# Performance work log

Measured on AMD Instinct MI355X. Metric: run time of the kernel, lower is better.

## Reference

```python
import jax, jax.numpy as jnp
import numpy as np

N = 50000        # nodes
E = 1600000      # edges (before self loops)
IN = 256         # in_channels
C = 32           # hidden_channels (per head)
H = 4            # heads
OUT = 64         # out_channels
NEG_SLOPE = 0.2  # PyG GATConv default


def setup_inputs() -> dict:
    key = jax.random.key(0)
    ks = jax.random.split(key, 8)
    x = jax.random.normal(ks[0], (N, IN), dtype=jnp.float32)
    edge_index = jax.random.randint(ks[1], (2, E), 0, N, dtype=jnp.int64)
    s = 0.05
    W = jax.random.normal(ks[2], (IN, H * C), dtype=jnp.float32) * s
    att_src = jax.random.normal(ks[3], (H, C), dtype=jnp.float32) * s
    att_dst = jax.random.normal(ks[4], (H, C), dtype=jnp.float32) * s
    bias = jnp.zeros((H * C,), dtype=jnp.float32)
    lin_W = jax.random.normal(ks[5], (H * C, OUT), dtype=jnp.float32) * s
    lin_b = jnp.zeros((OUT,), dtype=jnp.float32)
    return {"x": x, "edge_index": edge_index, "W": W, "att_src": att_src,
            "att_dst": att_dst, "bias": bias, "lin_W": lin_W, "lin_b": lin_b}


def reference(x, edge_index, W, att_src, att_dst, bias, lin_W, lin_b):
    # Linear transform per head: [N, H, C]
    h = (x @ W).reshape(N, H, C)
    # Per-node attention halves (PyG GATConv): [N, H]
    a_src = jnp.einsum('nhc,hc->nh', h, att_src)
    a_dst = jnp.einsum('nhc,hc->nh', h, att_dst)
    # Add self loops (PyG default add_self_loops=True)
    loop = jnp.arange(N, dtype=edge_index.dtype)
    src = jnp.concatenate([edge_index[0], loop])  # message source j
    dst = jnp.concatenate([edge_index[1], loop])  # message target i
    # Edge attention logits: LeakyReLU(a_src[j] + a_dst[i])  -> [E+N, H]
    e = jax.nn.leaky_relu(a_src[src] + a_dst[dst], negative_slope=NEG_SLOPE)
    # Segment softmax over incoming edges of each destination node
    emax = jax.lax.stop_gradient(jax.ops.segment_max(e, dst, num_segments=N))
    emax = jnp.where(jnp.isfinite(emax), emax, 0.0)
    ex = jnp.exp(e - emax[dst])
    denom = jax.ops.segment_sum(ex, dst, num_segments=N)
    alpha = ex / denom[dst]  # [E+N, H]; self loops guarantee denom > 0
    # Weighted scatter-sum of source features: [N, H, C]
    msg = alpha[:, :, None] * h[src]
    agg = jax.ops.segment_sum(msg, dst, num_segments=N)
    out = agg.reshape(N, H * C) + bias  # concat heads + bias
    out = jax.nn.elu(out)
    return out @ lin_W + lin_b
```

## Files before the change

kernel.cpp:

```cpp
#include <hip/hip_runtime.h>
#include <cstdint>
#include <cstddef>

#define N_NODES 50000
#define N_EDGES 1600000
#define TOT_E   (N_EDGES + N_NODES)
#define IN_DIM  256
#define HC      128
#define NHEAD   4
#define OUT_DIM 64

#define SHIFT   7
#define BSZ     128
#define NBUK    ((N_NODES + BSZ - 1) / BSZ)
#define CHUNK   2048
#define EPT     8
#define NCHUNK  ((TOT_E + CHUNK - 1) / CHUNK)
#define CAP     6144
#define QCAP    1792

#define XPAD 264
#define HPAD 132
#define K1_NB ((N_NODES + 63) / 64)

typedef __attribute__((ext_vector_type(8))) short bf16x8;
typedef __attribute__((ext_vector_type(4))) float f32x4;

static __device__ __forceinline__ uint16_t f2bf(float f) {
    uint32_t u = __float_as_uint(f);
    uint32_t r = (u + 0x7fffu + ((u >> 16) & 1u)) >> 16;
    return (uint16_t)r;
}
static __device__ __forceinline__ float bf_lo(uint32_t u) {
    return __uint_as_float(u << 16);
}
static __device__ __forceinline__ float bf_hi(uint32_t u) {
    return __uint_as_float(u & 0xffff0000u);
}

__global__ __launch_bounds__(256) void w2bf(const float* __restrict__ W,
                                            uint16_t* __restrict__ wt,
                                            int* __restrict__ gcur) {
    int idx = blockIdx.x * 256 + threadIdx.x;
    int n = idx >> 8, k = idx & 255;
    wt[idx] = f2bf(W[(size_t)k * HC + n]);
    if (idx < NBUK) gcur[idx] = 0;
}

__global__ __launch_bounds__(256) void k1p3(const float* __restrict__ x,
                                            const uint16_t* __restrict__ wt,
                                            const float* __restrict__ att_src,
                                            const float* __restrict__ att_dst,
                                            uint16_t* __restrict__ hb,
                                            float* __restrict__ a_src,
                                            float* __restrict__ a_dst,
                                            const int* __restrict__ ei,
                                            int* __restrict__ gcur,
                                            uint32_t* __restrict__ binned) {
    __shared__ char smem[64 * 528];
    __shared__ float att_s[HC], att_d[HC];
    const int tid = threadIdx.x;

    if (blockIdx.x < K1_NB) {
        uint16_t* xs = (uint16_t*)smem;
        float*    hs = (float*)smem;
        const int wave = tid >> 6;
        const int lane = tid & 63;
        const int m    = lane & 15;
        const int q    = lane >> 4;
        const int row0 = blockIdx.x * 64;

        if (tid < HC) { att_s[tid] = att_src[tid]; att_d[tid] = att_dst[tid]; }

        for (int i = tid * 4; i < 64 * IN_DIM; i += 1024) {
            int r = i >> 8, c = i & 255;
            int gr = row0 + r;
            float4 v = make_float4(0.f, 0.f, 0.f, 0.f);
            if (gr < N_NODES) v = *(const float4*)(x + (size_t)gr * IN_DIM + c);
            uint32_t lo = (uint32_t)f2bf(v.x) | ((uint32_t)f2bf(v.y) << 16);
            uint32_t hi = (uint32_t)f2bf(v.z) | ((uint32_t)f2bf(v.w) << 16);
            *(uint2*)(xs + r * XPAD + c) = make_uint2(lo, hi);
        }
        __syncthreads();

        f32x4 acc[8];
        #pragma unroll
        for (int t = 0; t < 8; ++t) acc[t] = (f32x4){0.f, 0.f, 0.f, 0.f};

        const int arow = wave * 16 + m;
        #pragma unroll
        for (int ks = 0; ks < IN_DIM; ks += 32) {
            bf16x8 a = *(const bf16x8*)(xs + arow * XPAD + ks + q * 8);
            #pragma unroll
            for (int t = 0; t < 8; ++t) {
                bf16x8 b = *(const bf16x8*)(wt + (size_t)(t * 16 + m) * IN_DIM + ks + q * 8);
                acc[t] = __builtin_amdgcn_mfma_f32_16x16x32_bf16(a, b, acc[t], 0, 0, 0);
            }
        }
        __syncthreads();

        #pragma unroll
        for (int t = 0; t < 8; ++t)
            #pragma unroll
            for (int r = 0; r < 4; ++r)
                hs[(wave * 16 + q * 4 + r) * HPAD + t * 16 + m] = acc[t][r];
        __syncthreads();

        for (int i = tid * 4; i < 64 * HC; i += 1024) {
            int r = i >> 7, c = i & 127;
            if (row0 + r < N_NODES) {
                float4 v = *(const float4*)(hs + r * HPAD + c);
                uint32_t lo = (uint32_t)f2bf(v.x) | ((uint32_t)f2bf(v.y) << 16);
                uint32_t hi = (uint32_t)f2bf(v.z) | ((uint32_t)f2bf(v.w) << 16);
                *(uint2*)(hb + (size_t)(row0 + r) * HC + c) = make_uint2(lo, hi);
            }
        }
        {
            int r = tid >> 2, hd = tid & 3;
            if (row0 + r < N_NODES) {
                float s = 0.f, d = 0.f;
                #pragma unroll
                for (int j = 0; j < 32; ++j) {
                    float v = hs[r * HPAD + hd * 32 + j];
                    s = fmaf(v, att_s[hd * 32 + j], s);
                    d = fmaf(v, att_d[hd * 32 + j], d);
                }
                a_src[(row0 + r) * NHEAD + hd] = s;
                a_dst[(row0 + r) * NHEAD + hd] = d;
            }
        }
    } else {
        int* hist = (int*)smem;
        int* lcur = hist + NBUK;
        for (int i = tid; i < NBUK; i += 256) hist[i] = 0;
        __syncthreads();

        uint32_t wreg[EPT];
        const int base = (blockIdx.x - K1_NB) * CHUNK;
        #pragma unroll
        for (int k = 0; k < EPT; ++k) {
            int e = base + k * 256 + tid;
            uint32_t word = 0xFFFFFFFFu;
            if (e < TOT_E) {
                int src, dst;
                if (e < N_EDGES) { src = ei[e]; dst = ei[N_EDGES + e]; }
                else             { src = e - N_EDGES; dst = src; }
                int b = dst >> SHIFT;
                word = (uint32_t)src | ((uint32_t)(dst & (BSZ - 1)) << 16)
                     | ((uint32_t)b << 23);
                atomicAdd(&hist[b], 1);
            }
            wreg[k] = word;
        }
        __syncthreads();
        for (int i = tid; i < NBUK; i += 256) {
            int c = hist[i];
            lcur[i] = c ? atomicAdd(&gcur[i], c) : 0;
        }
        __syncthreads();
        #pragma unroll
        for (int k = 0; k < EPT; ++k) {
            uint32_t word = wreg[k];
            if (word != 0xFFFFFFFFu) {
                int b = (int)(word >> 23);
                int pos = atomicAdd(&lcur[b], 1);
                if (pos < CAP) binned[(size_t)b * CAP + pos] = word;
            }
        }
    }
}

__global__ __launch_bounds__(256) void q4_agg(const uint32_t* __restrict__ binned,
                                              const int* __restrict__ gcur,
                                              const uint32_t* __restrict__ hb32,
                                              const float* __restrict__ a_src,
                                              const float* __restrict__ a_dst,
                                              const float* __restrict__ bias,
                                              uint32_t* __restrict__ actb) {
    __shared__ uint32_t ewb[QCAP];
    __shared__ uint32_t ew2[QCAP];
    __shared__ int ncnt[32], nbeg[32], ncur[32];
    __shared__ int tot;
    const int b   = blockIdx.x >> 2;
    const int sub = blockIdx.x & 3;
    const int tid = threadIdx.x;

    int cnt = gcur[b];
    if (cnt > CAP) cnt = CAP;
    if (tid == 0) tot = 0;
    if (tid < 32) ncnt[tid] = 0;
    __syncthreads();

    const uint32_t* bb = binned + (size_t)b * CAP;
    for (int i = tid; i < cnt; i += 256) {
        uint32_t word = bb[i];
        int dl = (word >> 16) & 127;
        if ((dl >> 5) == sub) {
            int pos = atomicAdd(&tot, 1);
            if (pos < QCAP) ewb[pos] = word;
            atomicAdd(&ncnt[dl & 31], 1);
        }
    }
    __syncthreads();
    int T = tot;
    if (T > QCAP) T = QCAP;

    if (tid < 32) {
        int v = ncnt[tid];
        int inc = v;
        #pragma unroll
        for (int d = 1; d < 32; d <<= 1) {
            int t = __shfl_up(inc, d, 64);
            if (tid >= d) inc += t;
        }
        nbeg[tid] = inc - v;
        ncur[tid] = inc - v;
    }
    __syncthreads();
    for (int i = tid; i < T; i += 256) {
        uint32_t word = ewb[i];
        int ln  = (word >> 16) & 31;
        int pos = atomicAdd(&ncur[ln], 1);
        ew2[pos] = word & 0xFFFFu;
    }
    __syncthreads();

    const int wave = tid >> 6;
    const int lane = tid & 63;
    const int head = lane >> 4;
    const uint32_t* hbl = hb32 + lane;
    const float*    ash = a_src + head;

    for (int k = 0; k < 8; ++k) {
        const int ln   = wave * 8 + k;
        const int node = b * BSZ + sub * 32 + ln;
        if (node >= N_NODES) continue;

        const float ad = a_dst[node * NHEAD + head];
        int p = nbeg[ln];
        const int end = p + ncnt[ln];

        float l = 0.f, acc0 = 0.f, acc1 = 0.f;

        for (; p + 4 <= end; p += 4) {
            int s0 = (int)ew2[p + 0];
            int s1 = (int)ew2[p + 1];
            int s2 = (int)ew2[p + 2];
            int s3 = (int)ew2[p + 3];
            float e0 = ash[s0 * NHEAD] + ad;
            float e1 = ash[s1 * NHEAD] + ad;
            float e2 = ash[s2 * NHEAD] + ad;
            float e3 = ash[s3 * NHEAD] + ad;
            uint32_t u0 = hbl[(size_t)s0 * 64];
            uint32_t u1 = hbl[(size_t)s1 * 64];
            uint32_t u2 = hbl[(size_t)s2 * 64];
            uint32_t u3 = hbl[(size_t)s3 * 64];
            e0 = fmaxf(e0, 0.2f * e0);
            e1 = fmaxf(e1, 0.2f * e1);
            e2 = fmaxf(e2, 0.2f * e2);
            e3 = fmaxf(e3, 0.2f * e3);
            float w0 = __expf(e0), w1 = __expf(e1);
            float w2 = __expf(e2), w3 = __expf(e3);
            l += (w0 + w1) + (w2 + w3);
            acc0 = fmaf(w0, bf_lo(u0), acc0);
            acc1 = fmaf(w0, bf_hi(u0), acc1);
            acc0 = fmaf(w1, bf_lo(u1), acc0);
            acc1 = fmaf(w1, bf_hi(u1), acc1);
            acc0 = fmaf(w2, bf_lo(u2), acc0);
            acc1 = fmaf(w2, bf_hi(u2), acc1);
            acc0 = fmaf(w3, bf_lo(u3), acc0);
            acc1 = fmaf(w3, bf_hi(u3), acc1);
        }
        for (; p < end; ++p) {
            int s = (int)ew2[p];
            float e = ash[s * NHEAD] + ad;
            e = fmaxf(e, 0.2f * e);
            float w = __expf(e);
            uint32_t u = hbl[(size_t)s * 64];
            l += w;
            acc0 = fmaf(w, bf_lo(u), acc0);
            acc1 = fmaf(w, bf_hi(u), acc1);
        }

        const int c0 = lane << 1;
        float inv = 1.f / l;
        float o0 = acc0 * inv + bias[c0];
        float o1 = acc1 * inv + bias[c0 + 1];
        o0 = (o0 > 0.f) ? o0 : (__expf(o0) - 1.f);
        o1 = (o1 > 0.f) ? o1 : (__expf(o1) - 1.f);
        actb[(size_t)node * 64 + lane] = (uint32_t)f2bf(o0) | ((uint32_t)f2bf(o1) << 16);
    }
}

__global__ __launch_bounds__(512) void k7_out(const uint32_t* __restrict__ actb,
                                              const float* __restrict__ linW,
                                              const float* __restrict__ linb,
                                              float* __restrict__ out) {
    __shared__ float sW[HC * OUT_DIM];
    __shared__ float srow[32 * HC];
    const int tid   = threadIdx.x;
    const int node0 = blockIdx.x * 32;

    for (int i = tid * 4; i < HC * OUT_DIM; i += 512 * 4)
        *(float4*)(sW + i) = *(const float4*)(linW + i);
    {
        int i = tid * 4;
        int r = i >> 6, cw = i & 63;
        int node = node0 + r;
        uint4 v = make_uint4(0, 0, 0, 0);
        if (node < N_NODES) v = *(const uint4*)(actb + (size_t)node * 64 + cw);
        float* d = srow + r * HC + cw * 2;
        d[0] = bf_lo(v.x); d[1] = bf_hi(v.x);
        d[2] = bf_lo(v.y); d[3] = bf_hi(v.y);
        d[4] = bf_lo(v.z); d[5] = bf_hi(v.z);
        d[6] = bf_lo(v.w); d[7] = bf_hi(v.w);
    }
    __syncthreads();

    const int r    = tid >> 4;
    const int colb = (tid & 15) << 2;
    float4 acc = *(const float4*)(linb + colb);
    const float* rp = srow + r * HC;

    #pragma unroll
    for (int k = 0; k < HC; k += 4) {
        float4 xv = *(const float4*)(rp + k);
        float4 w0 = *(const float4*)(sW + (k + 0) * OUT_DIM + colb);
        float4 w1 = *(const float4*)(sW + (k + 1) * OUT_DIM + colb);
        float4 w2 = *(const float4*)(sW + (k + 2) * OUT_DIM + colb);
        float4 w3 = *(const float4*)(sW + (k + 3) * OUT_DIM + colb);
        acc.x += xv.x * w0.x; acc.x += xv.y * w1.x; acc.x += xv.z * w2.x; acc.x += xv.w * w3.x;
        acc.y += xv.x * w0.y; acc.y += xv.y * w1.y; acc.y += xv.z * w2.y; acc.y += xv.w * w3.y;
        acc.z += xv.x * w0.z; acc.z += xv.y * w1.z; acc.z += xv.z * w2.z; acc.z += xv.w * w3.z;
        acc.w += xv.x * w0.w; acc.w += xv.y * w1.w; acc.w += xv.z * w2.w; acc.w += xv.w * w3.w;
    }

    int node = node0 + r;
    if (node < N_NODES)
        *(float4*)(out + (size_t)node * OUT_DIM + colb) = acc;
}

extern "C" void kernel_launch(void* const* d_in, const int* in_sizes, int n_in,
                              void* d_out, int out_size, void* d_ws, size_t ws_size,
                              hipStream_t stream) {
    (void)in_sizes; (void)n_in; (void)out_size; (void)ws_size;
    const float* x       = (const float*)d_in[0];
    const int*   ei      = (const int*)d_in[1];
    const float* W       = (const float*)d_in[2];
    const float* att_src = (const float*)d_in[3];
    const float* att_dst = (const float*)d_in[4];
    const float* bias    = (const float*)d_in[5];
    const float* linW    = (const float*)d_in[6];
    const float* linb    = (const float*)d_in[7];
    float*       out     = (float*)d_out;

    char*  ws  = (char*)d_ws;
    size_t off = 0;
    auto alloc = [&](size_t bytes) -> void* {
        void* p = ws + off;
        off += (bytes + 255) & ~(size_t)255;
        return p;
    };
    uint16_t* hb     = (uint16_t*)alloc((size_t)N_NODES * HC * 2);
    uint16_t* wt     = (uint16_t*)alloc((size_t)HC * IN_DIM * 2);
    uint32_t* actb   = (uint32_t*)alloc((size_t)N_NODES * 64 * 4);
    float*    a_src  = (float*)alloc((size_t)N_NODES * NHEAD * 4);
    float*    a_dst  = (float*)alloc((size_t)N_NODES * NHEAD * 4);
    int*      gcur   = (int*)alloc((size_t)NBUK * 4);
    uint32_t* binned = (uint32_t*)alloc((size_t)NBUK * CAP * 4);

    w2bf<<<(HC * IN_DIM) / 256, 256, 0, stream>>>(W, wt, gcur);
    k1p3<<<K1_NB + NCHUNK, 256, 0, stream>>>(x, wt, att_src, att_dst,
                                             hb, a_src, a_dst,
                                             ei, gcur, binned);
    q4_agg<<<NBUK * 4, 256, 0, stream>>>(binned, gcur, (const uint32_t*)hb,
                                         a_src, a_dst, bias, actb);
    k7_out<<<(N_NODES + 31) / 32, 512, 0, stream>>>(actb, linW, linb, out);
}
```

Measured before the change: 248.8 us.

## Vectorize aggregation per lane across 4 nodes and use MFMA for output linear

The aggregation kernel now processes four destination nodes per wave at once: each 16-lane group owns a node and each lane gathers 16 bytes (8 bf16 channels) per source, with edge lists padded to multiples of 4 and masked weights instead of a scalar tail loop. Source indices are stored as 16-bit values so four can be read with one LDS load. The final linear layer is rewritten to use bf16 MFMA 16x16x32 with linW split into hi and lo bf16 parts to keep near-fp32 accuracy, replacing the scalar FP32 LDS GEMM. The trade-offs are divergence, since every group runs to the wave's maximum degree, and extra weight preprocessing work in w2bf.

```diff
diff --git a/kernel.cpp b/kernel.cpp
--- a/kernel.cpp
+++ b/kernel.cpp
@@ -23,8 +23,12 @@
 #define HPAD 132
 #define K1_NB ((N_NODES + 63) / 64)
 
+#define W2_GEMM_BLK ((HC * IN_DIM) / 256)
+#define W2_LIN_BLK  ((OUT_DIM * HC) / 256)
+
 typedef __attribute__((ext_vector_type(8))) short bf16x8;
 typedef __attribute__((ext_vector_type(4))) float f32x4;
+typedef __attribute__((ext_vector_type(4))) unsigned short u16x4;
 
 static __device__ __forceinline__ uint16_t f2bf(float f) {
     uint32_t u = __float_as_uint(f);
@@ -39,12 +43,24 @@
 }
 
 __global__ __launch_bounds__(256) void w2bf(const float* __restrict__ W,
+                                            const float* __restrict__ linW,
                                             uint16_t* __restrict__ wt,
+                                            uint16_t* __restrict__ lwt,
                                             int* __restrict__ gcur) {
-    int idx = blockIdx.x * 256 + threadIdx.x;
-    int n = idx >> 8, k = idx & 255;
-    wt[idx] = f2bf(W[(size_t)k * HC + n]);
-    if (idx < NBUK) gcur[idx] = 0;
+    if (blockIdx.x < W2_GEMM_BLK) {
+        int idx = blockIdx.x * 256 + threadIdx.x;
+        int n = idx >> 8, k = idx & 255;
+        wt[idx] = f2bf(W[(size_t)k * HC + n]);
+        if (idx < NBUK) gcur[idx] = 0;
+    } else {
+        int idx = (blockIdx.x - W2_GEMM_BLK) * 256 + threadIdx.x;
+        int n = idx >> 7, k = idx & 127;
+        float w = linW[(size_t)k * OUT_DIM + n];
+        uint16_t h = f2bf(w);
+        float hf = __uint_as_float((uint32_t)h << 16);
+        lwt[idx] = h;
+        lwt[OUT_DIM * HC + idx] = f2bf(w - hf);
+    }
 }
 
 __global__ __launch_bounds__(256) void k1p3(const float* __restrict__ x,
@@ -178,7 +194,7 @@
                                               const float* __restrict__ bias,
                                               uint32_t* __restrict__ actb) {
     __shared__ uint32_t ewb[QCAP];
-    __shared__ uint32_t ew2[QCAP];
+    __shared__ uint16_t ew2[QCAP * 2];
     __shared__ int ncnt[32], nbeg[32], ncur[32];
     __shared__ int tot;
     const int b   = blockIdx.x >> 2;
@@ -206,138 +222,161 @@
     if (T > QCAP) T = QCAP;
 
     if (tid < 32) {
-        int v = ncnt[tid];
-        int inc = v;
+        int v  = ncnt[tid];
+        int v4 = (v + 3) & ~3;
+        int inc = v4;
         #pragma unroll
         for (int d = 1; d < 32; d <<= 1) {
             int t = __shfl_up(inc, d, 64);
             if (tid >= d) inc += t;
         }
-        nbeg[tid] = inc - v;
-        ncur[tid] = inc - v;
+        nbeg[tid] = inc - v4;
+        ncur[tid] = inc - v4;
     }
     __syncthreads();
     for (int i = tid; i < T; i += 256) {
         uint32_t word = ewb[i];
         int ln  = (word >> 16) & 31;
         int pos = atomicAdd(&ncur[ln], 1);
-        ew2[pos] = word & 0xFFFFu;
+        ew2[pos] = (uint16_t)(word & 0xFFFFu);
     }
     __syncthreads();
 
     const int wave = tid >> 6;
     const int lane = tid & 63;
-    const int head = lane >> 4;
-    const uint32_t* hbl = hb32 + lane;
-    const float*    ash = a_src + head;
-
-    for (int k = 0; k < 8; ++k) {
-        const int ln   = wave * 8 + k;
+    const int g    = lane >> 4;
+    const int sl   = lane & 15;
+    const int head = sl >> 2;
+    const char*  hb8 = (const char*)hb32 + sl * 16;
+    const float* ash = a_src + head;
+    const float4 bA = *(const float4*)(bias + sl * 8);
+    const float4 bB = *(const float4*)(bias + sl * 8 + 4);
+
+    for (int pass = 0; pass < 2; ++pass) {
+        const int ln   = wave * 8 + pass * 4 + g;
         const int node = b * BSZ + sub * 32 + ln;
-        if (node >= N_NODES) continue;
-
-        const float ad = a_dst[node * NHEAD + head];
-        int p = nbeg[ln];
-        const int end = p + ncnt[ln];
-
-        float l = 0.f, acc0 = 0.f, acc1 = 0.f;
-
-        for (; p + 4 <= end; p += 4) {
-            int s0 = (int)ew2[p + 0];
-            int s1 = (int)ew2[p + 1];
-            int s2 = (int)ew2[p + 2];
-            int s3 = (int)ew2[p + 3];
-            float e0 = ash[s0 * NHEAD] + ad;
-            float e1 = ash[s1 * NHEAD] + ad;
-            float e2 = ash[s2 * NHEAD] + ad;
-            float e3 = ash[s3 * NHEAD] + ad;
-            uint32_t u0 = hbl[(size_t)s0 * 64];
-            uint32_t u1 = hbl[(size_t)s1 * 64];
-            uint32_t u2 = hbl[(size_t)s2 * 64];
-            uint32_t u3 = hbl[(size_t)s3 * 64];
+        const int myc  = ncnt[ln];
+        const int p0   = nbeg[ln];
+        int m1   = max(myc, __shfl_xor(myc, 16, 64));
+        int maxc = max(m1,  __shfl_xor(m1, 32, 64));
+        const float ad = a_dst[min(node, N_NODES - 1) * NHEAD + head];
+
+        float l = 0.f;
+        float acc[8];
+        #pragma unroll
+        for (int j = 0; j < 8; ++j) acc[j] = 0.f;
+
+        for (int i = 0; i < maxc; i += 4) {
+            u16x4 sv = *(const u16x4*)(&ew2[p0 + i]);
+            const int s0 = sv[0], s1 = sv[1], s2 = sv[2], s3 = sv[3];
+            float as0 = ash[s0 * NHEAD];
+            float as1 = ash[s1 * NHEAD];
+            float as2 = ash[s2 * NHEAD];
+            float as3 = ash[s3 * NHEAD];
+            uint4 h0 = *(const uint4*)(hb8 + ((uint32_t)s0 << 8));
+            uint4 h1 = *(const uint4*)(hb8 + ((uint32_t)s1 << 8));
+            uint4 h2 = *(const uint4*)(hb8 + ((uint32_t)s2 << 8));
+            uint4 h3 = *(const uint4*)(hb8 + ((uint32_t)s3 << 8));
+            float e0 = as0 + ad, e1 = as1 + ad, e2 = as2 + ad, e3 = as3 + ad;
             e0 = fmaxf(e0, 0.2f * e0);
             e1 = fmaxf(e1, 0.2f * e1);
             e2 = fmaxf(e2, 0.2f * e2);
             e3 = fmaxf(e3, 0.2f * e3);
             float w0 = __expf(e0), w1 = __expf(e1);
             float w2 = __expf(e2), w3 = __expf(e3);
+            w0 = (i + 0 < myc) ? w0 : 0.f;
+            w1 = (i + 1 < myc) ? w1 : 0.f;
+            w2 = (i + 2 < myc) ? w2 : 0.f;
+            w3 = (i + 3 < myc) ? w3 : 0.f;
             l += (w0 + w1) + (w2 + w3);
-            acc0 = fmaf(w0, bf_lo(u0), acc0);
-            acc1 = fmaf(w0, bf_hi(u0), acc1);
-            acc0 = fmaf(w1, bf_lo(u1), acc0);
-            acc1 = fmaf(w1, bf_hi(u1), acc1);
-            acc0 = fmaf(w2, bf_lo(u2), acc0);
-            acc1 = fmaf(w2, bf_hi(u2), acc1);
-            acc0 = fmaf(w3, bf_lo(u3), acc0);
-            acc1 = fmaf(w3, bf_hi(u3), acc1);
-        }
-        for (; p < end; ++p) {
-            int s = (int)ew2[p];
-            float e = ash[s * NHEAD] + ad;
-            e = fmaxf(e, 0.2f * e);
-            float w = __expf(e);
-            uint32_t u = hbl[(size_t)s * 64];
-            l += w;
-            acc0 = fmaf(w, bf_lo(u), acc0);
-            acc1 = fmaf(w, bf_hi(u), acc1);
-        }
-
-        const int c0 = lane << 1;
-        float inv = 1.f / l;
-        float o0 = acc0 * inv + bias[c0];
-        float o1 = acc1 * inv + bias[c0 + 1];
-        o0 = (o0 > 0.f) ? o0 : (__expf(o0) - 1.f);
-        o1 = (o1 > 0.f) ? o1 : (__expf(o1) - 1.f);
-        actb[(size_t)node * 64 + lane] = (uint32_t)f2bf(o0) | ((uint32_t)f2bf(o1) << 16);
-    }
-}
-
-__global__ __launch_bounds__(512) void k7_out(const uint32_t* __restrict__ actb,
-                                              const float* __restrict__ linW,
+            acc[0] = fmaf(w0, bf_lo(h0.x), acc[0]); acc[0] = fmaf(w1, bf_lo(h1.x), acc[0]);
+            acc[0] = fmaf(w2, bf_lo(h2.x), acc[0]); acc[0] = fmaf(w3, bf_lo(h3.x), acc[0]);
+            acc[1] = fmaf(w0, bf_hi(h0.x), acc[1]); acc[1] = fmaf(w1, bf_hi(h1.x), acc[1]);
+            acc[1] = fmaf(w2, bf_hi(h2.x), acc[1]); acc[1] = fmaf(w3, bf_hi(h3.x), acc[1]);
+            acc[2] = fmaf(w0, bf_lo(h0.y), acc[2]); acc[2] = fmaf(w1, bf_lo(h1.y), acc[2]);
+            acc[2] = fmaf(w2, bf_lo(h2.y), acc[2]); acc[2] = fmaf(w3, bf_lo(h3.y), acc[2]);
+            acc[3] = fmaf(w0, bf_hi(h0.y), acc[3]); acc[3] = fmaf(w1, bf_hi(h1.y), acc[3]);
+            acc[3] = fmaf(w2, bf_hi(h2.y), acc[3]); acc[3] = fmaf(w3, bf_hi(h3.y), acc[3]);
+            acc[4] = fmaf(w0, bf_lo(h0.z), acc[4]); acc[4] = fmaf(w1, bf_lo(h1.z), acc[4]);
+            acc[4] = fmaf(w2, bf_lo(h2.z), acc[4]); acc[4] = fmaf(w3, bf_lo(h3.z), acc[4]);
+            acc[5] = fmaf(w0, bf_hi(h0.z), acc[5]); acc[5] = fmaf(w1, bf_hi(h1.z), acc[5]);
+            acc[5] = fmaf(w2, bf_hi(h2.z), acc[5]); acc[5] = fmaf(w3, bf_hi(h3.z), acc[5]);
+            acc[6] = fmaf(w0, bf_lo(h0.w), acc[6]); acc[6] = fmaf(w1, bf_lo(h1.w), acc[6]);
+            acc[6] = fmaf(w2, bf_lo(h2.w), acc[6]); acc[6] = fmaf(w3, bf_lo(h3.w), acc[6]);
+            acc[7] = fmaf(w0, bf_hi(h0.w), acc[7]); acc[7] = fmaf(w1, bf_hi(h1.w), acc[7]);
+            acc[7] = fmaf(w2, bf_hi(h2.w), acc[7]); acc[7] = fmaf(w3, bf_hi(h3.w), acc[7]);
+        }
+
+        if (node < N_NODES) {
+            const float inv = 1.f / l;
+            float o[8];
+            o[0] = fmaf(acc[0], inv, bA.x); o[1] = fmaf(acc[1], inv, bA.y);
+            o[2] = fmaf(acc[2], inv, bA.z); o[3] = fmaf(acc[3], inv, bA.w);
+            o[4] = fmaf(acc[4], inv, bB.x); o[5] = fmaf(acc[5], inv, bB.y);
+            o[6] = fmaf(acc[6], inv, bB.z); o[7] = fmaf(acc[7], inv, bB.w);
+            #pragma unroll
+            for (int j = 0; j < 8; ++j)
+                o[j] = (o[j] > 0.f) ? o[j] : (__expf(o[j]) - 1.f);
+            uint4 pk;
+            pk.x = (uint32_t)f2bf(o[0]) | ((uint32_t)f2bf(o[1]) << 16);
+            pk.y = (uint32_t)f2bf(o[2]) | ((uint32_t)f2bf(o[3]) << 16);
+            pk.z = (uint32_t)f2bf(o[4]) | ((uint32_t)f2bf(o[5]) << 16);
+            pk.w = (uint32_t)f2bf(o[6]) | ((uint32_t)f2bf(o[7]) << 16);
+            *(uint4*)(actb + (size_t)node * 64 + sl * 4) = pk;
+        }
+    }
+}
+
+__global__ __launch_bounds__(256) void k7_out(const uint16_t* __restrict__ ab,
+                                              const uint16_t* __restrict__ lwt,
                                               const float* __restrict__ linb,
                                               float* __restrict__ out) {
-    __shared__ float sW[HC * OUT_DIM];
-    __shared__ float srow[32 * HC];
-    const int tid   = threadIdx.x;
-    const int node0 = blockIdx.x * 32;
-
-    for (int i = tid * 4; i < HC * OUT_DIM; i += 512 * 4)
-        *(float4*)(sW + i) = *(const float4*)(linW + i);
-    {
-        int i = tid * 4;
-        int r = i >> 6, cw = i & 63;
-        int node = node0 + r;
+    __shared__ uint16_t as_[64][136];
+    const int tid  = threadIdx.x;
+    const int row0 = blockIdx.x * 64;
+
+    for (int i = tid; i < 64 * 16; i += 256) {
+        int r = i >> 4, cw = i & 15;
+        int node = row0 + r;
         uint4 v = make_uint4(0, 0, 0, 0);
-        if (node < N_NODES) v = *(const uint4*)(actb + (size_t)node * 64 + cw);
-        float* d = srow + r * HC + cw * 2;
-        d[0] = bf_lo(v.x); d[1] = bf_hi(v.x);
-        d[2] = bf_lo(v.y); d[3] = bf_hi(v.y);
-        d[4] = bf_lo(v.z); d[5] = bf_hi(v.z);
-        d[6] = bf_lo(v.w); d[7] = bf_hi(v.w);
+        if (node < N_NODES) v = *(const uint4*)(ab + (size_t)node * HC + cw * 8);
+        *(uint4*)(&as_[r][cw * 8]) = v;
     }
     __syncthreads();
 
-    const int r    = tid >> 4;
-    const int colb = (tid & 15) << 2;
-    float4 acc = *(const float4*)(linb + colb);
-    const float* rp = srow + r * HC;
-
+    const int wave = tid >> 6;
+    const int lane = tid & 63;
+    const int m    = lane & 15;
+    const int q    = lane >> 4;
+    const uint16_t* lwlo = lwt + OUT_DIM * HC;
+
+    f32x4 acc[4];
     #pragma unroll
-    for (int k = 0; k < HC; k += 4) {
-        float4 xv = *(const float4*)(rp + k);
-        float4 w0 = *(const float4*)(sW + (k + 0) * OUT_DIM + colb);
-        float4 w1 = *(const float4*)(sW + (k + 1) * OUT_DIM + colb);
-        float4 w2 = *(const float4*)(sW + (k + 2) * OUT_DIM + colb);
-        float4 w3 = *(const float4*)(sW + (k + 3) * OUT_DIM + colb);
-        acc.x += xv.x * w0.x; acc.x += xv.y * w1.x; acc.x += xv.z * w2.x; acc.x += xv.w * w3.x;
-        acc.y += xv.x * w0.y; acc.y += xv.y * w1.y; acc.y += xv.z * w2.y; acc.y += xv.w * w3.y;
-        acc.z += xv.x * w0.z; acc.z += xv.y * w1.z; acc.z += xv.z * w2.z; acc.z += xv.w * w3.z;
-        acc.w += xv.x * w0.w; acc.w += xv.y * w1.w; acc.w += xv.z * w2.w; acc.w += xv.w * w3.w;
-    }
-
-    int node = node0 + r;
-    if (node < N_NODES)
-        *(float4*)(out + (size_t)node * OUT_DIM + colb) = acc;
+    for (int t = 0; t < 4; ++t) acc[t] = (f32x4){0.f, 0.f, 0.f, 0.f};
+
+    const int arow = wave * 16 + m;
+    #pragma unroll
+    for (int ks = 0; ks < HC; ks += 32) {
+        bf16x8 a = *(const bf16x8*)(&as_[arow][ks + q * 8]);
+        #pragma unroll
+        for (int t = 0; t < 4; ++t) {
+            bf16x8 bh = *(const bf16x8*)(lwt  + (size_t)(t * 16 + m) * HC + ks + q * 8);
+            bf16x8 bl = *(const bf16x8*)(lwlo + (size_t)(t * 16 + m) * HC + ks + q * 8);
+            acc[t] = __builtin_amdgcn_mfma_f32_16x16x32_bf16(a, bh, acc[t], 0, 0, 0);
+            acc[t] = __builtin_amdgcn_mfma_f32_16x16x32_bf16(a, bl, acc[t], 0, 0, 0);
+        }
+    }
+
+    const int grow = row0 + wave * 16 + q * 4;
+    #pragma unroll
+    for (int t = 0; t < 4; ++t) {
+        const int col = t * 16 + m;
+        const float lb = linb[col];
+        #pragma unroll
+        for (int r = 0; r < 4; ++r)
+            if (grow + r < N_NODES)
+                out[(size_t)(grow + r) * OUT_DIM + col] = acc[t][r] + lb;
+    }
 }
 
 extern "C" void kernel_launch(void* const* d_in, const int* in_sizes, int n_in,
@@ -368,12 +407,14 @@
     float*    a_dst  = (float*)alloc((size_t)N_NODES * NHEAD * 4);
     int*      gcur   = (int*)alloc((size_t)NBUK * 4);
     uint32_t* binned = (uint32_t*)alloc((size_t)NBUK * CAP * 4);
-
-    w2bf<<<(HC * IN_DIM) / 256, 256, 0, stream>>>(W, wt, gcur);
+    uint16_t* lwt    = (uint16_t*)alloc((size_t)2 * OUT_DIM * HC * 2);
+
+    w2bf<<<W2_GEMM_BLK + W2_LIN_BLK, 256, 0, stream>>>(W, linW, wt, lwt, gcur);
     k1p3<<<K1_NB + NCHUNK, 256, 0, stream>>>(x, wt, att_src, att_dst,
                                              hb, a_src, a_dst,
                                              ei, gcur, binned);
     q4_agg<<<NBUK * 4, 256, 0, stream>>>(binned, gcur, (const uint32_t*)hb,
                                          a_src, a_dst, bias, actb);
-    k7_out<<<(N_NODES + 31) / 32, 512, 0, stream>>>(actb, linW, linb, out);
-}
+    k7_out<<<(N_NODES + 63) / 64, 256, 0, stream>>>((const uint16_t*)actb, lwt,
+                                                    linb, out);
+}
```

Measured after the change: 239.2 us. 1.04x faster.
